# Optimization experiments

Measured on AMD Instinct MI355X. Metric: run time of the kernel, lower is better.

## Reference

```python
import jax, jax.numpy as jnp
import numpy as np

NW, NT, ND, D = 30000, 2000, 20000, 128
E = {'ww': 600000, 'wt': 300000, 'wd': 400000, 'td': 100000, 'tt': 40000}
ENDS = {'ww': (NW, NW), 'wt': (NW, NT), 'wd': (NW, ND), 'td': (NT, ND), 'tt': (NT, NT)}


def setup_inputs() -> dict:
    key = jax.random.key(0)
    ks = iter(jax.random.split(key, 64))
    nrm = lambda shape: jax.random.normal(next(ks), shape, dtype=jnp.float32)
    inp = {}
    inp['feat_word'] = nrm((NW, D))
    inp['feat_topic'] = nrm((NT, D))
    # 'effect' node data: ~half the topics are causal (nonzero effect)
    inp['effect'] = jax.random.randint(next(ks), (NT,), 0, 2).astype(jnp.float32)
    # independent Bernoulli(0.1) draws for the td and tt iterations
    inp['bern_td'] = (jax.random.uniform(next(ks), (NT,)) < 0.1).astype(jnp.float32)
    inp['bern_tt'] = (jax.random.uniform(next(ks), (NT,)) < 0.1).astype(jnp.float32)
    for et, (ns, nd) in ENDS.items():
        inp[f'src_{et}'] = jax.random.randint(next(ks), (E[et],), 0, ns, dtype=jnp.int32)
        inp[f'dst_{et}'] = jax.random.randint(next(ks), (E[et],), 0, nd, dtype=jnp.int32)
        inp[f'w_{et}'] = jax.random.uniform(next(ks), (E[et],), dtype=jnp.float32)
    for name in ['ww', 'wt', 'wd', 'td', 'tt']:
        inp[f'W_{name}'] = nrm((D, D)) * 0.05
        inp[f'b_{name}'] = jnp.zeros((D,), jnp.float32)
    inp['W_causal'] = nrm((D, D)) * 0.05
    inp['W_noise'] = nrm((D, D)) * 0.05
    inp['n_doc'] = ND
    return inp


def _mean_agg(Wh, w, src, dst, n_dst):
    # DGL fn.u_mul_e + fn.mean: mean of (Wh[src]*w) over incoming edges; 0 for isolated dst
    m = Wh[src] * w[:, None]                                    # [E, D]
    s = jax.ops.segment_sum(m, dst, num_segments=n_dst)          # [n_dst, D]
    deg = jax.ops.segment_sum(jnp.ones_like(w), dst, num_segments=n_dst)
    return jnp.where(deg[:, None] > 0, s / jnp.maximum(deg, 1.0)[:, None], 0.0)


def reference(feat_word, feat_topic, effect, bern_td, bern_tt,
              src_ww, dst_ww, w_ww, src_wt, dst_wt, w_wt,
              src_wd, dst_wd, w_wd, src_td, dst_td, w_td,
              src_tt, dst_tt, w_tt,
              W_ww, b_ww, W_wt, b_wt, W_wd, b_wd, W_td, b_td, W_tt, b_tt,
              W_causal, W_noise, n_doc):
    n_word, n_topic = feat_word.shape[0], feat_topic.shape[0]
    # Phase 1: word -> word (ww)
    h_word = _mean_agg(feat_word @ W_ww + b_ww, w_ww, src_ww, dst_ww, n_word)
    # Phase 2: remaining etypes; word features replaced by h
    causal = (effect != 0).astype(feat_topic.dtype)[:, None]     # [NT, 1]
    rm_td = (bern_td * (effect == 0))[:, None]
    rm_tt = (bern_tt * (effect == 0))[:, None]
    Wh_wt = h_word @ W_wt + b_wt
    Wh_wd = h_word @ W_wd + b_wd
    Wh_td = (feat_topic @ W_td + b_td
             + (feat_topic * causal) @ W_causal - (feat_topic * rm_td) @ W_noise)
    Wh_tt = (feat_topic @ W_tt + b_tt
             + (feat_topic * causal) @ W_causal - (feat_topic * rm_tt) @ W_noise)
    # cross-relation 'sum' reducer per destination ntype
    h_topic = (_mean_agg(Wh_wt, w_wt, src_wt, dst_wt, n_topic)
               + _mean_agg(Wh_tt, w_tt, src_tt, dst_tt, n_topic))
    h_doc = (_mean_agg(Wh_wd, w_wd, src_wd, dst_wd, n_doc)
             + _mean_agg(Wh_td, w_td, src_td, dst_td, n_doc))
    return h_word, h_topic, h_doc
```

## Files before the change

### kernel.cpp

```cpp
#include <hip/hip_runtime.h>

#define D 128
typedef unsigned short u16;
constexpr int NW = 30000;
constexpr int NT = 2000;
constexpr int NDOC = 20000;

constexpr int CAPB = 1024;
constexpr int SSP  = 136;
constexpr int NBK_WW = (NW + 31) / 32;
constexpr int NBK_WT = NT / 4;
constexpr int NBK_TT = (NT + 31) / 32;
constexpr int NBK_WD = (NDOC + 31) / 32;
constexpr int NBK_TD = (NDOC + 31) / 32;
constexpr int BUK_WW = 0;
constexpr int BUK_WT = BUK_WW + NBK_WW;
constexpr int BUK_TT = BUK_WT + NBK_WT;
constexpr int BUK_WD = BUK_TT + NBK_TT;
constexpr int BUK_TD = BUK_WD + NBK_WD;
constexpr int NBUK   = BUK_TD + NBK_TD;

constexpr int EPB = 4096;
constexpr int NF2B = (NW * D / 4 + 255) / 256;
constexpr int NBM4 = (NT + 63) / 64;

struct RelDesc { const int* src; const int* dst; const float* w;
                 int e0; int buk0; int shift; int mask; };
struct Rels { RelDesc r[5]; };

__device__ __forceinline__ int which_rel(const Rels& R, int e)
{
    if (e < R.r[1].e0) return 0;
    if (e < R.r[2].e0) return 1;
    if (e < R.r[3].e0) return 2;
    if (e < R.r[4].e0) return 3;
    return 4;
}

__device__ __forceinline__ float b2f(u16 h)
{
    return __uint_as_float(((unsigned)h) << 16);
}
__device__ __forceinline__ u16 f2b(float f)
{
    unsigned u = __float_as_uint(f);
    return (u16)((u + 0x7FFF + ((u >> 16) & 1)) >> 16);
}

typedef short bf16x8 __attribute__((ext_vector_type(8)));
typedef float f32x4 __attribute__((ext_vector_type(4)));
constexpr int WPITCH = 136;

__device__ __forceinline__ void stage_wt(
    const float* __restrict__ Wg, u16* Wt, int tid)
{
    for (int i = tid; i < D * D; i += 256) {
        int k = i >> 7, nn = i & 127;
        Wt[nn * WPITCH + k] = f2b(Wg[i]);
    }
}

__device__ __forceinline__ void mfma_tile_f32(
    const float* __restrict__ X, const u16* Wt, int arow, int n,
    int lanelo, int quad, f32x4 acc[8])
{
#pragma unroll
    for (int ct = 0; ct < 8; ++ct) {
        acc[ct][0] = 0.f; acc[ct][1] = 0.f; acc[ct][2] = 0.f; acc[ct][3] = 0.f;
    }
#pragma unroll
    for (int k0 = 0; k0 < 4; ++k0) {
        bf16x8 a;
        if (arow < n) {
            const float* ap = X + (size_t)arow * D + k0 * 32 + quad * 8;
            float4 a0 = *(const float4*)ap;
            float4 a1 = *(const float4*)(ap + 4);
            a[0] = (short)f2b(a0.x); a[1] = (short)f2b(a0.y);
            a[2] = (short)f2b(a0.z); a[3] = (short)f2b(a0.w);
            a[4] = (short)f2b(a1.x); a[5] = (short)f2b(a1.y);
            a[6] = (short)f2b(a1.z); a[7] = (short)f2b(a1.w);
        } else {
#pragma unroll
            for (int j = 0; j < 8; ++j) a[j] = 0;
        }
#pragma unroll
        for (int ct = 0; ct < 8; ++ct) {
            bf16x8 b = *(const bf16x8*)&Wt[(ct * 16 + lanelo) * WPITCH
                                           + k0 * 32 + quad * 8];
            acc[ct] = __builtin_amdgcn_mfma_f32_16x16x32_bf16(a, b, acc[ct], 0, 0, 0);
        }
    }
}

struct MM4 { const float* W[4]; float* P[4]; };
struct TR3 { const float* W[3]; u16* T[3]; };

__global__ __launch_bounds__(256) void prep_kernel(
    const float* __restrict__ feat_word, u16* __restrict__ fw16,
    const float* __restrict__ feat_topic, MM4 m4, TR3 tr, int* __restrict__ cur)
{
    __shared__ u16 Wt[D * WPITCH];
    int tid = threadIdx.x;

    if ((int)blockIdx.x < NF2B) {
        int i = blockIdx.x * 256 + tid;
        if (i < NW * D / 4) {
            float4 v = ((const float4*)feat_word)[i];
            ushort4 o;
            o.x = f2b(v.x); o.y = f2b(v.y); o.z = f2b(v.z); o.w = f2b(v.w);
            ((ushort4*)fw16)[i] = o;
        }
    } else if ((int)blockIdx.x < NF2B + 4 * NBM4) {
        int idx = blockIdx.x - NF2B;
        int which = idx / NBM4;
        int bx = idx % NBM4;
        stage_wt(m4.W[which], Wt, tid);
        __syncthreads();
        int wv = tid >> 6, lane = tid & 63;
        int lanelo = lane & 15, quad = lane >> 4;
        int rowbase = bx * 64 + wv * 16;
        f32x4 acc[8];
        mfma_tile_f32(feat_topic, Wt, rowbase + lanelo, NT, lanelo, quad, acc);
        float* Y = m4.P[which];
        int rbase = rowbase + quad * 4;
#pragma unroll
        for (int r = 0; r < 4; ++r) {
            int row = rbase + r;
            if (row >= NT) continue;
#pragma unroll
            for (int ct = 0; ct < 8; ++ct)
                Y[(size_t)row * D + ct * 16 + lanelo] = acc[ct][r];
        }
    } else if ((int)blockIdx.x < NF2B + 4 * NBM4 + 3) {
        int which = blockIdx.x - NF2B - 4 * NBM4;
        stage_wt(tr.W[which], Wt, tid);
        __syncthreads();
        u16* Wd = tr.T[which];
        for (int i = tid; i < D * D; i += 256) {
            int nrow = i >> 7, k = i & 127;
            Wd[i] = Wt[nrow * WPITCH + k];
        }
    } else {
        for (int i = tid; i < NBUK; i += 256) cur[i] = 0;
    }
}

__global__ __launch_bounds__(256) void part_combine_kernel(
    Rels R, int Etot, int* __restrict__ cur, int2* __restrict__ edataP,
    const float* __restrict__ P_td, const float* __restrict__ P_tt,
    const float* __restrict__ Pc, const float* __restrict__ Pn,
    const float* __restrict__ effect, const float* __restrict__ bern_td,
    const float* __restrict__ bern_tt,
    const float* __restrict__ b_td, const float* __restrict__ b_tt,
    u16* __restrict__ wtd16, u16* __restrict__ wtt16, int npb)
{
    __shared__ int hist[NBUK];
    __shared__ int baseL[NBUK];
    int tid = threadIdx.x;

    if ((int)blockIdx.x >= npb) {
        int i = ((int)blockIdx.x - npb) * 256 + tid;
        if (i < NT * D) {
            int row = i >> 7;
            int col = i & (D - 1);
            float eff = effect[row];
            float causal = (eff != 0.f) ? 1.f : 0.f;
            float zero = (eff == 0.f) ? 1.f : 0.f;
            float rmtd = bern_td[row] * zero;
            float rmtt = bern_tt[row] * zero;
            float pc = Pc[i];
            float pn = Pn[i];
            wtd16[i] = f2b(P_td[i] + b_td[col] + causal * pc - rmtd * pn);
            wtt16[i] = f2b(P_tt[i] + b_tt[col] + causal * pc - rmtt * pn);
        }
        return;
    }

    for (int i = tid; i < NBUK; i += 256) hist[i] = 0;
    __syncthreads();
    int base_e = blockIdx.x * EPB;
    int bs[EPB / 256];
    int2 se[EPB / 256];
#pragma unroll
    for (int r = 0; r < EPB / 256; ++r) {
        int e = base_e + r * 256 + tid;
        if (e < Etot) {
            int k = which_rel(R, e);
            int le = e - R.r[k].e0;
            int s = R.r[k].src[le];
            int dd = R.r[k].dst[le];
            float w = R.r[k].w[le];
            int b = R.r[k].buk0 + (dd >> R.r[k].shift);
            int dloc = dd & R.r[k].mask;
            bs[r] = b;
            se[r] = make_int2(s | (dloc << 15), __float_as_int(w));
            atomicAdd(&hist[b], 1);
        } else {
            bs[r] = -1;
        }
    }
    __syncthreads();
    for (int i = tid; i < NBUK; i += 256)
        baseL[i] = hist[i] ? atomicAdd(&cur[i], hist[i]) : 0;
    __syncthreads();
    for (int i = tid; i < NBUK; i += 256) hist[i] = 0;
    __syncthreads();
#pragma unroll
    for (int r = 0; r < EPB / 256; ++r) {
        int b = bs[r];
        if (b >= 0) {
            int rk = atomicAdd(&hist[b], 1) + baseL[b];
            if (rk < CAPB)
                edataP[(size_t)b * CAPB + rk] = se[r];
        }
    }
}

struct BucketSmem {
    int2 st[CAPB];
    u16  ord[CAPB];
    u16  Ssum[32 * SSP];
    float degL[32];
    float wsumL[32];
    int h2[32], exc[32], cnt[32];
};

__device__ __forceinline__ void reduce_one_lds(
    const u16* __restrict__ Xb, const int2* st, const u16* ord,
    int start, int end, int dl, int lane, BucketSmem& s)
{
    int half = lane >> 5;
    int q = (lane & 31) * 4;
    float4 acc = make_float4(0.f, 0.f, 0.f, 0.f);
    float wacc = 0.f;
    int j = start;
    for (; j + 16 <= end; j += 16) {
        int2 ee[8];
        ushort4 vv[8];
#pragma unroll
        for (int t = 0; t < 8; ++t) ee[t] = st[ord[j + 2 * t + half]];
#pragma unroll
        for (int t = 0; t < 8; ++t)
            vv[t] = *(const ushort4*)(Xb + (size_t)(ee[t].x & 0x7FFF) * D + q);
#pragma unroll
        for (int t = 0; t < 8; ++t) {
            float w = __int_as_float(ee[t].y);
            acc.x = fmaf(w, b2f(vv[t].x), acc.x);
            acc.y = fmaf(w, b2f(vv[t].y), acc.y);
            acc.z = fmaf(w, b2f(vv[t].z), acc.z);
            acc.w = fmaf(w, b2f(vv[t].w), acc.w);
            wacc += w;
        }
    }
    if (j + 8 <= end) {
        int2 ee[4];
        ushort4 vv[4];
#pragma unroll
        for (int t = 0; t < 4; ++t) ee[t] = st[ord[j + 2 * t + half]];
#pragma unroll
        for (int t = 0; t < 4; ++t)
            vv[t] = *(const ushort4*)(Xb + (size_t)(ee[t].x & 0x7FFF) * D + q);
#pragma unroll
        for (int t = 0; t < 4; ++t) {
            float w = __int_as_float(ee[t].y);
            acc.x = fmaf(w, b2f(vv[t].x), acc.x);
            acc.y = fmaf(w, b2f(vv[t].y), acc.y);
            acc.z = fmaf(w, b2f(vv[t].z), acc.z);
            acc.w = fmaf(w, b2f(vv[t].w), acc.w);
            wacc += w;
        }
        j += 8;
    }
    if (j + 4 <= end) {
        int2 ea = st[ord[j + half]];
        int2 eb = st[ord[j + 2 + half]];
        ushort4 va = *(const ushort4*)(Xb + (size_t)(ea.x & 0x7FFF) * D + q);
        ushort4 vb = *(const ushort4*)(Xb + (size_t)(eb.x & 0x7FFF) * D + q);
        float wa = __int_as_float(ea.y);
        float wb = __int_as_float(eb.y);
        acc.x = fmaf(wa, b2f(va.x), acc.x); acc.y = fmaf(wa, b2f(va.y), acc.y);
        acc.z = fmaf(wa, b2f(va.z), acc.z); acc.w = fmaf(wa, b2f(va.w), acc.w);
        acc.x = fmaf(wb, b2f(vb.x), acc.x); acc.y = fmaf(wb, b2f(vb.y), acc.y);
        acc.z = fmaf(wb, b2f(vb.z), acc.z); acc.w = fmaf(wb, b2f(vb.w), acc.w);
        wacc += wa + wb;
        j += 4;
    }
    for (; j < end; j += 2) {
        int jj = j + half;
        int2 e = st[ord[jj < end ? jj : (end - 1)]];
        float w = (jj < end) ? __int_as_float(e.y) : 0.f;
        ushort4 v = *(const ushort4*)(Xb + (size_t)(e.x & 0x7FFF) * D + q);
        acc.x = fmaf(w, b2f(v.x), acc.x); acc.y = fmaf(w, b2f(v.y), acc.y);
        acc.z = fmaf(w, b2f(v.z), acc.z); acc.w = fmaf(w, b2f(v.w), acc.w);
        wacc += w;
    }
    acc.x += __shfl_xor(acc.x, 32);
    acc.y += __shfl_xor(acc.y, 32);
    acc.z += __shfl_xor(acc.z, 32);
    acc.w += __shfl_xor(acc.w, 32);
    wacc  += __shfl_xor(wacc, 32);
    if (half == 0) {
        ushort4 o;
        o.x = f2b(acc.x); o.y = f2b(acc.y); o.z = f2b(acc.z); o.w = f2b(acc.w);
        *(ushort4*)(s.Ssum + dl * SSP + q) = o;
    }
    if (lane == 0) {
        s.degL[dl] = (float)(end - start);
        s.wsumL[dl] = wacc;
    }
}

__device__ __forceinline__ void bucket_reduce(
    const u16* __restrict__ X, const int* __restrict__ cur,
    const int2* __restrict__ edataP, int buk, int nsl, BucketSmem& s)
{
    int tid = threadIdx.x;
    int nE = min(cur[buk], CAPB);
    const int2* gsrc = edataP + (size_t)buk * CAPB;
    for (int i = tid; i < nE; i += 256) s.st[i] = gsrc[i];
    if (tid < 32) { s.h2[tid] = 0; s.cnt[tid] = 0; }
    __syncthreads();
    for (int i = tid; i < nE; i += 256)
        atomicAdd(&s.h2[(s.st[i].x >> 15) & 31], 1);
    __syncthreads();
    if (tid < 32) s.exc[tid] = s.h2[tid];
    __syncthreads();
    for (int off = 1; off < 32; off <<= 1) {
        int t = 0;
        if (tid < 32 && tid >= off) t = s.exc[tid - off];
        __syncthreads();
        if (tid < 32) s.exc[tid] += t;
        __syncthreads();
    }
    if (tid < 32) s.exc[tid] -= s.h2[tid];
    __syncthreads();
    for (int i = tid; i < nE; i += 256) {
        int dl = (s.st[i].x >> 15) & 31;
        int rk = atomicAdd(&s.cnt[dl], 1);
        s.ord[s.exc[dl] + rk] = (u16)i;
    }
    __syncthreads();
    int wv = tid >> 6, lane = tid & 63;
    for (int dl = wv; dl < nsl; dl += 4) {
        int start = s.exc[dl];
        reduce_one_lds(X, s.st, s.ord, start, start + s.h2[dl], dl, lane, s);
    }
}

__device__ __forceinline__ void fused_mm(
    BucketSmem& s, const u16* __restrict__ Wtg, const float* __restrict__ bias,
    const u16* __restrict__ Tg, const float* __restrict__ degTg,
    float* __restrict__ Y, u16* __restrict__ Yb, int row0, int n, int tid)
{
    int wv = tid >> 6, lane = tid & 63;
    int lanelo = lane & 15, quad = lane >> 4;
    int rt = wv >> 1, ch = wv & 1;
    int arow = rt * 16 + lanelo;
    f32x4 acc[4];
#pragma unroll
    for (int c = 0; c < 4; ++c) {
        acc[c][0] = 0.f; acc[c][1] = 0.f; acc[c][2] = 0.f; acc[c][3] = 0.f;
    }
#pragma unroll
    for (int k0 = 0; k0 < 4; ++k0) {
        bf16x8 a;
        if (arow < n) {
            a = *(const bf16x8*)(s.Ssum + arow * SSP + k0 * 32 + quad * 8);
        } else {
#pragma unroll
            for (int j = 0; j < 8; ++j) a[j] = 0;
        }
#pragma unroll
        for (int c = 0; c < 4; ++c) {
            int ct = ch * 4 + c;
            bf16x8 b = *(const bf16x8*)(Wtg + (ct * 16 + lanelo) * D
                                        + k0 * 32 + quad * 8);
            acc[c] = __builtin_amdgcn_mfma_f32_16x16x32_bf16(a, b, acc[c], 0, 0, 0);
        }
    }
    int rbase = rt * 16 + quad * 4;
#pragma unroll
    for (int r = 0; r < 4; ++r) {
        int row = rbase + r;
        if (row >= n) continue;
        float dgv = s.degL[row];
        float wsv = s.wsumL[row];
        float dtv = degTg ? degTg[row] : 0.f;
#pragma unroll
        for (int c = 0; c < 4; ++c) {
            int ct = ch * 4 + c;
            int col = ct * 16 + lanelo;
            float y = acc[c][r];
            y = dgv > 0.f ? (y + wsv * bias[col]) / dgv : 0.f;
            if (Tg && dtv > 0.f) y += b2f(Tg[(size_t)row * D + col]) / dtv;
            Y[(size_t)(row0 + row) * D + col] = y;
            if (Yb) Yb[(size_t)(row0 + row) * D + col] = f2b(y);
        }
    }
}

__device__ __forceinline__ void dump_smem(
    BucketSmem& s, u16* __restrict__ Sg, float* __restrict__ degg,
    int nsl, int tid)
{
    for (int i = tid; i < nsl * 32; i += 256) {
        int row = i >> 5, c4 = (i & 31) * 4;
        *(ushort4*)(Sg + (size_t)row * D + c4) =
            *(const ushort4*)(s.Ssum + row * SSP + c4);
    }
    if (tid < nsl) degg[tid] = s.degL[tid];
}

__global__ __launch_bounds__(256, 8) void phaseA_kernel(
    const u16* __restrict__ fw16, const u16* __restrict__ wtt16,
    const u16* __restrict__ wtd16, const int* __restrict__ cur,
    const int2* __restrict__ edataP,
    const u16* __restrict__ Wtg_ww, const float* __restrict__ b_ww,
    float* __restrict__ h_word, u16* __restrict__ hw16,
    u16* __restrict__ Sb2, float* __restrict__ degf2)
{
    __shared__ BucketSmem s;
    int b = blockIdx.x;
    int tid = threadIdx.x;
    if (b < NBK_WW) {
        int w0 = b * 32;
        int nsl = min(32, NW - w0);
        bucket_reduce(fw16, cur, edataP, BUK_WW + b, nsl, s);
        __syncthreads();
        fused_mm(s, Wtg_ww, b_ww, nullptr, nullptr, h_word, hw16, w0, nsl, tid);
    } else if (b < NBK_WW + NBK_TT) {
        int i = b - NBK_WW;
        int t0 = i * 32;
        int nsl = min(32, NT - t0);
        bucket_reduce(wtt16, cur, edataP, BUK_TT + i, nsl, s);
        __syncthreads();
        dump_smem(s, Sb2 + (size_t)t0 * D, degf2 + t0, nsl, tid);
    } else {
        int i = b - NBK_WW - NBK_TT;
        int d0 = i * 32;
        int nsl = min(32, NDOC - d0);
        bucket_reduce(wtd16, cur, edataP, BUK_TD + i, nsl, s);
        __syncthreads();
        dump_smem(s, Sb2 + (size_t)(NT + d0) * D, degf2 + NT + d0, nsl, tid);
    }
}

__global__ __launch_bounds__(256, 8) void phaseB_kernel(
    const u16* __restrict__ hw16, const int* __restrict__ cur,
    const int2* __restrict__ edataP,
    const u16* __restrict__ Wtg_wt, const float* __restrict__ b_wt,
    const u16* __restrict__ Wtg_wd, const float* __restrict__ b_wd,
    const u16* __restrict__ Sb2, const float* __restrict__ degf2,
    float* __restrict__ h_topic, float* __restrict__ h_doc)
{
    __shared__ BucketSmem s;
    int b = blockIdx.x;
    int tid = threadIdx.x;
    if (b < NBK_WT) {
        int t0 = b * 4;
        bucket_reduce(hw16, cur, edataP, BUK_WT + b, 4, s);
        __syncthreads();
        fused_mm(s, Wtg_wt, b_wt, Sb2 + (size_t)t0 * D, degf2 + t0,
                 h_topic, nullptr, t0, 4, tid);
    } else {
        int i = b - NBK_WT;
        int d0 = i * 32;
        int nsl = min(32, NDOC - d0);
        bucket_reduce(hw16, cur, edataP, BUK_WD + i, nsl, s);
        __syncthreads();
        fused_mm(s, Wtg_wd, b_wd, Sb2 + (size_t)(NT + d0) * D, degf2 + NT + d0,
                 h_doc, nullptr, d0, nsl, tid);
    }
}

extern "C" void kernel_launch(void* const* d_in, const int* in_sizes, int n_in,
                              void* d_out, int out_size, void* d_ws, size_t ws_size,
                              hipStream_t stream)
{
    const float* feat_word  = (const float*)d_in[0];
    const float* feat_topic = (const float*)d_in[1];
    const float* effect     = (const float*)d_in[2];
    const float* bern_td    = (const float*)d_in[3];
    const float* bern_tt    = (const float*)d_in[4];
    const int*   src_ww = (const int*)d_in[5];
    const int*   dst_ww = (const int*)d_in[6];
    const float* w_ww   = (const float*)d_in[7];
    const int*   src_wt = (const int*)d_in[8];
    const int*   dst_wt = (const int*)d_in[9];
    const float* w_wt   = (const float*)d_in[10];
    const int*   src_wd = (const int*)d_in[11];
    const int*   dst_wd = (const int*)d_in[12];
    const float* w_wd   = (const float*)d_in[13];
    const int*   src_td = (const int*)d_in[14];
    const int*   dst_td = (const int*)d_in[15];
    const float* w_td   = (const float*)d_in[16];
    const int*   src_tt = (const int*)d_in[17];
    const int*   dst_tt = (const int*)d_in[18];
    const float* w_tt   = (const float*)d_in[19];
    const float* W_ww = (const float*)d_in[20];
    const float* b_ww = (const float*)d_in[21];
    const float* W_wt = (const float*)d_in[22];
    const float* b_wt = (const float*)d_in[23];
    const float* W_wd = (const float*)d_in[24];
    const float* b_wd = (const float*)d_in[25];
    const float* W_td = (const float*)d_in[26];
    const float* b_td = (const float*)d_in[27];
    const float* W_tt = (const float*)d_in[28];
    const float* b_tt = (const float*)d_in[29];
    const float* W_causal = (const float*)d_in[30];
    const float* W_noise  = (const float*)d_in[31];

    const int E_ww = in_sizes[5];
    const int E_wt = in_sizes[8];
    const int E_wd = in_sizes[11];
    const int E_td = in_sizes[14];
    const int E_tt = in_sizes[17];
    const int E_total = E_ww + E_wt + E_wd + E_td + E_tt;

    float* ws = (float*)d_ws;
    u16*   Sb2   = (u16*)ws; ws += (long long)(NT + NDOC) * D / 2;
    float* degf2 = ws; ws += NT + NDOC;
    int*   cur   = (int*)ws; ws += NBUK;
    ws += ((size_t)(ws - (float*)d_ws) & 1);
    int2*  edataP = (int2*)ws; ws += (long long)2 * NBUK * CAPB;
    float* P_td  = ws; ws += (long long)NT * D;
    float* P_tt  = ws; ws += (long long)NT * D;
    float* Pc    = ws; ws += (long long)NT * D;
    float* Pn    = ws; ws += (long long)NT * D;
    u16*   fw16  = (u16*)ws;  ws += (long long)NW * D / 2;
    u16*   hw16  = (u16*)ws;  ws += (long long)NW * D / 2;
    u16*   wtd16 = (u16*)ws;  ws += (long long)NT * D / 2;
    u16*   wtt16 = (u16*)ws;  ws += (long long)NT * D / 2;
    u16*   Wtg_ww = (u16*)ws; ws += (long long)D * D / 2;
    u16*   Wtg_wt = (u16*)ws; ws += (long long)D * D / 2;
    u16*   Wtg_wd = (u16*)ws; ws += (long long)D * D / 2;

    float* h_word  = (float*)d_out;
    float* h_topic = h_word + (long long)NW * D;
    float* h_doc   = h_topic + (long long)NT * D;

    auto nb = [](long long n) { return (unsigned)((n + 255) / 256); };

    Rels R;
    R.r[0] = { src_ww, dst_ww, w_ww, 0,                         BUK_WW, 5, 31 };
    R.r[1] = { src_wt, dst_wt, w_wt, E_ww,                      BUK_WT, 2, 3  };
    R.r[2] = { src_tt, dst_tt, w_tt, E_ww + E_wt,               BUK_TT, 5, 31 };
    R.r[3] = { src_wd, dst_wd, w_wd, E_ww + E_wt + E_tt,        BUK_WD, 5, 31 };
    R.r[4] = { src_td, dst_td, w_td, E_ww + E_wt + E_tt + E_wd, BUK_TD, 5, 31 };

    MM4 m4;
    m4.W[0] = W_td; m4.W[1] = W_tt; m4.W[2] = W_causal; m4.W[3] = W_noise;
    m4.P[0] = P_td; m4.P[1] = P_tt; m4.P[2] = Pc;       m4.P[3] = Pn;
    TR3 tr;
    tr.W[0] = W_ww; tr.W[1] = W_wt; tr.W[2] = W_wd;
    tr.T[0] = Wtg_ww; tr.T[1] = Wtg_wt; tr.T[2] = Wtg_wd;
    prep_kernel<<<NF2B + 4 * NBM4 + 3 + 1, 256, 0, stream>>>(
        feat_word, fw16, feat_topic, m4, tr, cur);

    unsigned npb = (unsigned)((E_total + EPB - 1) / EPB);
    part_combine_kernel<<<npb + nb((long long)NT * D), 256, 0, stream>>>(
        R, E_total, cur, edataP,
        P_td, P_tt, Pc, Pn, effect, bern_td, bern_tt, b_td, b_tt,
        wtd16, wtt16, (int)npb);

    phaseA_kernel<<<NBK_WW + NBK_TT + NBK_TD, 256, 0, stream>>>(
        fw16, wtt16, wtd16, cur, edataP, Wtg_ww, b_ww,
        h_word, hw16, Sb2, degf2);

    phaseB_kernel<<<NBK_WT + NBK_WD, 256, 0, stream>>>(
        hw16, cur, edataP, Wtg_wt, b_wt, Wtg_wd, b_wd,
        Sb2, degf2, h_topic, h_doc);

    (void)n_in; (void)in_sizes; (void)out_size; (void)ws_size;
}
```

Before: 249.0 us.

## Sort bucket edges directly into LDS and drop the index indirection

Edge records are now loaded into registers, and the counting sort scatters the full int2 records straight into the shared-memory edge array. This removes the separate u16 order array and the double indirection during the gather-reduce. The main reduction loop is also unrolled to 32 edges per iteration, giving more outstanding gathers. Launch bounds drop to 4 blocks per SM so the larger register footprint fits, which may reduce occupancy.

```diff
diff --git a/kernel.cpp b/kernel.cpp
--- a/kernel.cpp
+++ b/kernel.cpp
@@ -218,7 +218,6 @@
 
 struct BucketSmem {
     int2 st[CAPB];
-    u16  ord[CAPB];
     u16  Ssum[32 * SSP];
     float degL[32];
     float wsumL[32];
@@ -226,7 +225,7 @@
 };
 
 __device__ __forceinline__ void reduce_one_lds(
-    const u16* __restrict__ Xb, const int2* st, const u16* ord,
+    const u16* __restrict__ Xb, const int2* st,
     int start, int end, int dl, int lane, BucketSmem& s)
 {
     int half = lane >> 5;
@@ -234,11 +233,29 @@
     float4 acc = make_float4(0.f, 0.f, 0.f, 0.f);
     float wacc = 0.f;
     int j = start;
-    for (; j + 16 <= end; j += 16) {
+    for (; j + 32 <= end; j += 32) {
+        int2 ee[16];
+        ushort4 vv[16];
+#pragma unroll
+        for (int t = 0; t < 16; ++t) ee[t] = st[j + 2 * t + half];
+#pragma unroll
+        for (int t = 0; t < 16; ++t)
+            vv[t] = *(const ushort4*)(Xb + (size_t)(ee[t].x & 0x7FFF) * D + q);
+#pragma unroll
+        for (int t = 0; t < 16; ++t) {
+            float w = __int_as_float(ee[t].y);
+            acc.x = fmaf(w, b2f(vv[t].x), acc.x);
+            acc.y = fmaf(w, b2f(vv[t].y), acc.y);
+            acc.z = fmaf(w, b2f(vv[t].z), acc.z);
+            acc.w = fmaf(w, b2f(vv[t].w), acc.w);
+            wacc += w;
+        }
+    }
+    if (j + 16 <= end) {
         int2 ee[8];
         ushort4 vv[8];
 #pragma unroll
-        for (int t = 0; t < 8; ++t) ee[t] = st[ord[j + 2 * t + half]];
+        for (int t = 0; t < 8; ++t) ee[t] = st[j + 2 * t + half];
 #pragma unroll
         for (int t = 0; t < 8; ++t)
             vv[t] = *(const ushort4*)(Xb + (size_t)(ee[t].x & 0x7FFF) * D + q);
@@ -251,12 +268,13 @@
             acc.w = fmaf(w, b2f(vv[t].w), acc.w);
             wacc += w;
         }
+        j += 16;
     }
     if (j + 8 <= end) {
         int2 ee[4];
         ushort4 vv[4];
 #pragma unroll
-        for (int t = 0; t < 4; ++t) ee[t] = st[ord[j + 2 * t + half]];
+        for (int t = 0; t < 4; ++t) ee[t] = st[j + 2 * t + half];
 #pragma unroll
         for (int t = 0; t < 4; ++t)
             vv[t] = *(const ushort4*)(Xb + (size_t)(ee[t].x & 0x7FFF) * D + q);
@@ -272,8 +290,8 @@
         j += 8;
     }
     if (j + 4 <= end) {
-        int2 ea = st[ord[j + half]];
-        int2 eb = st[ord[j + 2 + half]];
+        int2 ea = st[j + half];
+        int2 eb = st[j + 2 + half];
         ushort4 va = *(const ushort4*)(Xb + (size_t)(ea.x & 0x7FFF) * D + q);
         ushort4 vb = *(const ushort4*)(Xb + (size_t)(eb.x & 0x7FFF) * D + q);
         float wa = __int_as_float(ea.y);
@@ -287,7 +305,7 @@
     }
     for (; j < end; j += 2) {
         int jj = j + half;
-        int2 e = st[ord[jj < end ? jj : (end - 1)]];
+        int2 e = st[jj < end ? jj : (end - 1)];
         float w = (jj < end) ? __int_as_float(e.y) : 0.f;
         ushort4 v = *(const ushort4*)(Xb + (size_t)(e.x & 0x7FFF) * D + q);
         acc.x = fmaf(w, b2f(v.x), acc.x); acc.y = fmaf(w, b2f(v.y), acc.y);
@@ -317,11 +335,19 @@
     int tid = threadIdx.x;
     int nE = min(cur[buk], CAPB);
     const int2* gsrc = edataP + (size_t)buk * CAPB;
-    for (int i = tid; i < nE; i += 256) s.st[i] = gsrc[i];
+    int2 ev[CAPB / 256];
+#pragma unroll
+    for (int t = 0; t < CAPB / 256; ++t) {
+        int i = t * 256 + tid;
+        if (i < nE) ev[t] = gsrc[i];
+    }
     if (tid < 32) { s.h2[tid] = 0; s.cnt[tid] = 0; }
     __syncthreads();
-    for (int i = tid; i < nE; i += 256)
-        atomicAdd(&s.h2[(s.st[i].x >> 15) & 31], 1);
+#pragma unroll
+    for (int t = 0; t < CAPB / 256; ++t) {
+        int i = t * 256 + tid;
+        if (i < nE) atomicAdd(&s.h2[(ev[t].x >> 15) & 31], 1);
+    }
     __syncthreads();
     if (tid < 32) s.exc[tid] = s.h2[tid];
     __syncthreads();
@@ -334,16 +360,20 @@
     }
     if (tid < 32) s.exc[tid] -= s.h2[tid];
     __syncthreads();
-    for (int i = tid; i < nE; i += 256) {
-        int dl = (s.st[i].x >> 15) & 31;
-        int rk = atomicAdd(&s.cnt[dl], 1);
-        s.ord[s.exc[dl] + rk] = (u16)i;
+#pragma unroll
+    for (int t = 0; t < CAPB / 256; ++t) {
+        int i = t * 256 + tid;
+        if (i < nE) {
+            int dl = (ev[t].x >> 15) & 31;
+            int rk = atomicAdd(&s.cnt[dl], 1);
+            s.st[s.exc[dl] + rk] = ev[t];
+        }
     }
     __syncthreads();
     int wv = tid >> 6, lane = tid & 63;
     for (int dl = wv; dl < nsl; dl += 4) {
         int start = s.exc[dl];
-        reduce_one_lds(X, s.st, s.ord, start, start + s.h2[dl], dl, lane, s);
+        reduce_one_lds(X, s.st, start, start + s.h2[dl], dl, lane, s);
     }
 }
 
@@ -411,7 +441,7 @@
     if (tid < nsl) degg[tid] = s.degL[tid];
 }
 
-__global__ __launch_bounds__(256, 8) void phaseA_kernel(
+__global__ __launch_bounds__(256, 4) void phaseA_kernel(
     const u16* __restrict__ fw16, const u16* __restrict__ wtt16,
     const u16* __restrict__ wtd16, const int* __restrict__ cur,
     const int2* __restrict__ edataP,
@@ -445,7 +475,7 @@
     }
 }
 
-__global__ __launch_bounds__(256, 8) void phaseB_kernel(
+__global__ __launch_bounds__(256, 4) void phaseB_kernel(
     const u16* __restrict__ hw16, const int* __restrict__ cur,
     const int2* __restrict__ edataP,
     const u16* __restrict__ Wtg_wt, const float* __restrict__ b_wt,
```

Measured after the change: 251.8 us. About the same (+1.1%).
